# Performance work log

Hardware: AMD Instinct MI355X
Metric: run time of the kernel (lower is better)

The kernel has to match this reference:

```python
import jax, jax.numpy as jnp
import numpy as np
from jax import lax

# NLM hyperparameters (from init_kwargs)
H_PARAM = 7.0 / 255.0          # OpenCV h is in 0-255 intensity units; images are in [0,1]
H2 = H_PARAM * H_PARAM
T = 7                          # template (patch) window size
TH = T // 2
S = 21                         # search window size
SH = S // 2


def setup_inputs() -> dict:
    key = jax.random.key(0)
    x = jax.random.uniform(key, (4, 1, 1024, 1024), dtype=jnp.float32)
    return {"x": x}


def _box_mean(d):
    # mean filter over TxT template window with reflect ('same') padding,
    # done as two separable 1D convolutions.
    k = (jnp.ones((T,), dtype=d.dtype) / T)
    dp = jnp.pad(d, ((0, 0), (0, 0), (TH, TH), (TH, TH)), mode="reflect")
    dn = ("NCHW", "OIHW", "NCHW")
    y = lax.conv_general_dilated(dp, k.reshape(1, 1, T, 1), (1, 1), "VALID", dimension_numbers=dn)
    y = lax.conv_general_dilated(y, k.reshape(1, 1, 1, T), (1, 1), "VALID", dimension_numbers=dn)
    return y


def reference(x):
    B, C, H, W = x.shape
    xc = jnp.clip(x, 0.0, 1.0)
    # reflect-pad by the search radius so every shift is a plain slice
    padded = jnp.pad(xc, ((0, 0), (0, 0), (SH, SH), (SH, SH)), mode="reflect")

    # all SxS = 441 search-window offsets, as padded-array slice origins in [0, 2*SH]
    oy, ox = jnp.meshgrid(jnp.arange(S, dtype=jnp.int32), jnp.arange(S, dtype=jnp.int32), indexing="ij")
    offsets = jnp.stack([oy.reshape(-1), ox.reshape(-1)], axis=-1)  # [441, 2]

    zero = jnp.int32(0)

    def body(carry, off):
        wsum, vsum = carry
        shifted = lax.dynamic_slice(padded, (zero, zero, off[0], off[1]), (B, C, H, W))
        dist = _box_mean((xc - shifted) ** 2)          # mean squared patch difference
        w = jnp.exp(-dist / H2)                        # NLM similarity weight
        return (wsum + w, vsum + w * shifted), None

    init = (jnp.zeros_like(xc), jnp.zeros_like(xc))
    (wsum, vsum), _ = lax.scan(body, init, offsets)
    out = vsum / wsum
    return jnp.clip(out, 0.0, 1.0)
```

## Files before the change

kernel.cpp:

```cpp
#include <hip/hip_runtime.h>
#include <cstddef>


constexpr int TS    = 32;
constexpr int XSTR  = 61;
constexpr int XROWS = 59;
constexpr int XSZ   = XROWS * XSTR;
constexpr int VSTR  = 42;
constexpr int VROWS = 33;
constexpr int VS_SZ = VROWS * VSTR;

__device__ __forceinline__ int refl(int i, int n) {
    i = (i < 0) ? -i : i;
    return (i >= n) ? (2 * n - 2 - i) : i;
}

template<bool FASTROWS>
__device__ __forceinline__ void nlm_body(const float* __restrict__ img,
                                         float* __restrict__ out,
                                         int H, int W, int gx0, int gy0,
                                         float* xs, float* vsh, int tid)
{
    for (int e = tid; e < XSZ; e += 256) {
        int i = e / XSTR, j = e - i * XSTR;
        int jj = (j > 57) ? 57 : j;
        int gy = refl(gy0 - 13 + i, H);
        int gx = refl(gx0 - 13 + jj, W);
        float v = img[(size_t)gy * W + gx];
        xs[e] = fminf(fmaxf(v, 0.0f), 1.0f);
    }
    __syncthreads();

    const bool bv = (tid < 114);
    float u[17];
    int   aS[17];
    int   aB = 0;
    int   wb;
    {
        int t  = bv ? tid : 0;
        int g  = t / 38;
        int cc = t - g * 38;
        int r  = g * 11;
        int mxm10 = refl(gx0 + cc - 3, W) - gx0 + 3;
        if (FASTROWS) {
            aB = r * XSTR + mxm10;
#pragma unroll
            for (int i = 0; i < 17; ++i)
                u[i] = xs[(r + i + 10) * XSTR + mxm10 + 10];
        } else {
#pragma unroll
            for (int i = 0; i < 17; ++i) {
                int my = refl(gy0 + r + i - 3, H) - gy0 + 13;
                u[i]  = xs[my * XSTR + mxm10 + 10];
                aS[i] = (my - 10) * XSTR + mxm10;
            }
        }
        wb = r * VSTR + cc;
    }

    const bool cact = (tid >= 128);
    const int ct = cact ? (tid - 128) : 0;
    const int py = ct >> 2;
    const int c8 = (ct & 3) * 8;
    const int vb = py * VSTR + c8;
    int svC = (py + 3) * XSTR + (c8 + 3);

    int oxB = 0;
    int oxC = 0;

    float p[7];
    float ws[8], ac[8];
#pragma unroll
    for (int k = 0; k < 8; ++k) { ws[k] = 0.f; ac[k] = 0.f; }
    const float K = -(65025.0f / 2401.0f) * 1.4426950408889634f;

    auto bv_step = [&](int buf) {
        if (bv) {
            float* vo = vsh + buf * VS_SZ + wb;
            float q[17];
#pragma unroll
            for (int i = 0; i < 17; ++i) {
                float sh = FASTROWS ? xs[aB + i * XSTR] : xs[aS[i]];
                float d  = u[i] - sh;
                q[i] = d * d;
            }
            float s = ((q[0] + q[1]) + (q[2] + q[3])) + ((q[4] + q[5]) + q[6]);
            vo[0] = s;
#pragma unroll
            for (int k = 1; k < 11; ++k) {
                s += q[k + 6] - q[k - 1];
                vo[k * VSTR] = s;
            }
            int step = (oxB == 20) ? (XSTR - 20) : 1;
            if (FASTROWS) {
                aB += step;
            } else {
#pragma unroll
                for (int i = 0; i < 17; ++i) aS[i] += step;
            }
        }
        oxB = (oxB == 20) ? 0 : oxB + 1;
    };

    auto c_step = [&](int buf) {
        if (cact) {
            if (oxC == 0) {
#pragma unroll
                for (int k = 0; k < 7; ++k) p[k] = xs[svC + k];
            }
            const float2* vp =
                reinterpret_cast<const float2*>(vsh + buf * VS_SZ + vb);
            float2 tA = vp[0], tB = vp[1], tC = vp[2], tD = vp[3];
            float2 tE = vp[4], tF = vp[5], tG = vp[6];
            float p7 = xs[svC + 7 + oxC];
            float h0 = ((tA.x + tA.y) + (tB.x + tB.y)) + ((tC.x + tC.y) + tD.x);
            float h1 = h0 - tA.x + tD.y;
            float h2 = h1 - tA.y + tE.x;
            float h3 = h2 - tB.x + tE.y;
            float h4 = h3 - tB.y + tF.x;
            float h5 = h4 - tC.x + tF.y;
            float h6 = h5 - tC.y + tG.x;
            float h7 = h6 - tD.x + tG.y;
            float w;
            w = __builtin_amdgcn_exp2f(h0 * K); ws[0] += w; ac[0] = fmaf(w, p[0], ac[0]);
            w = __builtin_amdgcn_exp2f(h1 * K); ws[1] += w; ac[1] = fmaf(w, p[1], ac[1]);
            w = __builtin_amdgcn_exp2f(h2 * K); ws[2] += w; ac[2] = fmaf(w, p[2], ac[2]);
            w = __builtin_amdgcn_exp2f(h3 * K); ws[3] += w; ac[3] = fmaf(w, p[3], ac[3]);
            w = __builtin_amdgcn_exp2f(h4 * K); ws[4] += w; ac[4] = fmaf(w, p[4], ac[4]);
            w = __builtin_amdgcn_exp2f(h5 * K); ws[5] += w; ac[5] = fmaf(w, p[5], ac[5]);
            w = __builtin_amdgcn_exp2f(h6 * K); ws[6] += w; ac[6] = fmaf(w, p[6], ac[6]);
            w = __builtin_amdgcn_exp2f(h7 * K); ws[7] += w; ac[7] = fmaf(w, p7,   ac[7]);
#pragma unroll
            for (int k = 0; k < 6; ++k) p[k] = p[k + 1];
            p[6] = p7;
        }
        if (oxC == 20) { oxC = 0; svC += XSTR; } else { ++oxC; }
    };

    bv_step(0);
    __syncthreads();
#pragma unroll 1
    for (int i = 1; i < 441; ++i) {
        bv_step(i & 1);
        c_step(1 - (i & 1));
        __syncthreads();
    }
    c_step(0);

    if (cact) {
        float4 oA, oB;
        oA.x = fminf(fmaxf(ac[0] * __builtin_amdgcn_rcpf(ws[0]), 0.f), 1.f);
        oA.y = fminf(fmaxf(ac[1] * __builtin_amdgcn_rcpf(ws[1]), 0.f), 1.f);
        oA.z = fminf(fmaxf(ac[2] * __builtin_amdgcn_rcpf(ws[2]), 0.f), 1.f);
        oA.w = fminf(fmaxf(ac[3] * __builtin_amdgcn_rcpf(ws[3]), 0.f), 1.f);
        oB.x = fminf(fmaxf(ac[4] * __builtin_amdgcn_rcpf(ws[4]), 0.f), 1.f);
        oB.y = fminf(fmaxf(ac[5] * __builtin_amdgcn_rcpf(ws[5]), 0.f), 1.f);
        oB.z = fminf(fmaxf(ac[6] * __builtin_amdgcn_rcpf(ws[6]), 0.f), 1.f);
        oB.w = fminf(fmaxf(ac[7] * __builtin_amdgcn_rcpf(ws[7]), 0.f), 1.f);
        float* op = &out[((size_t)blockIdx.z * H + (gy0 + py)) * W + (gx0 + c8)];
        *reinterpret_cast<float4*>(op)     = oA;
        *reinterpret_cast<float4*>(op + 4) = oB;
    }
}

__global__ __launch_bounds__(256)
void nlm_kernel(const float* __restrict__ img_all, float* __restrict__ out,
                int H, int W) {
    __shared__ float xs[XSZ];
    __shared__ float vsh[2 * VS_SZ];
    const int tid = threadIdx.x;
    const int gx0 = blockIdx.x * TS;
    const int gy0 = blockIdx.y * TS;
    const float* img = img_all + (size_t)blockIdx.z * H * W;
    if (gy0 - 3 >= 0 && gy0 + 35 < H)
        nlm_body<true>(img, out, H, W, gx0, gy0, xs, vsh, tid);
    else
        nlm_body<false>(img, out, H, W, gx0, gy0, xs, vsh, tid);
}

extern "C" void kernel_launch(void* const* d_in, const int* in_sizes, int n_in,
                              void* d_out, int out_size, void* d_ws, size_t ws_size,
                              hipStream_t stream) {
    const float* x = (const float*)d_in[0];
    float* out = (float*)d_out;
    const int H = 1024, W = 1024;
    const int B = in_sizes[0] / (H * W);
    dim3 grid(W / TS, H / TS, B);
    nlm_kernel<<<grid, dim3(256), 0, stream>>>(x, out, H, W);
}
```

Baseline: 892.7 us.

## Pack vertical patch sums into float2 ops and prescale image to fold exp constant

The interior fast path now computes the vertical box sums for two adjacent columns per thread using 2-wide vector loads and arithmetic, halving the active producer threads and the LDS load instructions. The image is prescaled by sqrt of the exponent constant, which removes a multiply per weight, and the output is unscaled at the end. The XSTR padding changes to 62 to keep the float2 accesses aligned, and the fast path now also requires interior columns. The costs are possible new LDS bank conflicts from the new stride and slight floating-point rounding differences.

```diff
diff --git a/kernel.cpp b/kernel.cpp
--- a/kernel.cpp
+++ b/kernel.cpp
@@ -2,8 +2,10 @@
 #include <cstddef>
 
 
+typedef float v2f __attribute__((ext_vector_type(2)));
+
 constexpr int TS    = 32;
-constexpr int XSTR  = 61;
+constexpr int XSTR  = 62;
 constexpr int XROWS = 59;
 constexpr int XSZ   = XROWS * XSTR;
 constexpr int VSTR  = 42;
@@ -15,45 +17,51 @@
     return (i >= n) ? (2 * n - 2 - i) : i;
 }
 
-template<bool FASTROWS>
+template<bool FAST>
 __device__ __forceinline__ void nlm_body(const float* __restrict__ img,
                                          float* __restrict__ out,
                                          int H, int W, int gx0, int gy0,
                                          float* xs, float* vsh, int tid)
 {
+    const float NK  = (65025.0f / 2401.0f) * 1.4426950408889634f;
+    const float LAM = sqrtf(NK);
+
     for (int e = tid; e < XSZ; e += 256) {
         int i = e / XSTR, j = e - i * XSTR;
         int jj = (j > 57) ? 57 : j;
         int gy = refl(gy0 - 13 + i, H);
         int gx = refl(gx0 - 13 + jj, W);
         float v = img[(size_t)gy * W + gx];
-        xs[e] = fminf(fmaxf(v, 0.0f), 1.0f);
+        xs[e] = fminf(fmaxf(v, 0.0f), 1.0f) * LAM;
     }
     __syncthreads();
 
-    const bool bv = (tid < 114);
-    float u[17];
-    int   aS[17];
-    int   aB = 0;
-    int   wb;
-    {
+    const bool bv = FAST ? (tid < 57) : (tid < 114);
+    v2f   uP[17]; int aB = 0;
+    float uS[17]; int aS[17];
+    int   wb = 0;
+    if constexpr (FAST) {
+        int t  = bv ? tid : 0;
+        int g  = t / 19;
+        int pp = t - g * 19;
+        int r  = g * 11;
+        int cc = 2 * pp;
+        aB = r * XSTR + cc;
+        wb = r * VSTR + cc;
+#pragma unroll
+        for (int i = 0; i < 17; ++i)
+            uP[i] = *reinterpret_cast<const v2f*>(&xs[(r + i + 10) * XSTR + cc + 10]);
+    } else {
         int t  = bv ? tid : 0;
         int g  = t / 38;
         int cc = t - g * 38;
         int r  = g * 11;
         int mxm10 = refl(gx0 + cc - 3, W) - gx0 + 3;
-        if (FASTROWS) {
-            aB = r * XSTR + mxm10;
-#pragma unroll
-            for (int i = 0; i < 17; ++i)
-                u[i] = xs[(r + i + 10) * XSTR + mxm10 + 10];
-        } else {
-#pragma unroll
-            for (int i = 0; i < 17; ++i) {
-                int my = refl(gy0 + r + i - 3, H) - gy0 + 13;
-                u[i]  = xs[my * XSTR + mxm10 + 10];
-                aS[i] = (my - 10) * XSTR + mxm10;
-            }
+#pragma unroll
+        for (int i = 0; i < 17; ++i) {
+            int my = refl(gy0 + r + i - 3, H) - gy0 + 13;
+            uS[i] = xs[my * XSTR + mxm10 + 10];
+            aS[i] = (my - 10) * XSTR + mxm10;
         }
         wb = r * VSTR + cc;
     }
@@ -72,34 +80,51 @@
     float ws[8], ac[8];
 #pragma unroll
     for (int k = 0; k < 8; ++k) { ws[k] = 0.f; ac[k] = 0.f; }
-    const float K = -(65025.0f / 2401.0f) * 1.4426950408889634f;
 
     auto bv_step = [&](int buf) {
         if (bv) {
             float* vo = vsh + buf * VS_SZ + wb;
-            float q[17];
-#pragma unroll
-            for (int i = 0; i < 17; ++i) {
-                float sh = FASTROWS ? xs[aB + i * XSTR] : xs[aS[i]];
-                float d  = u[i] - sh;
-                q[i] = d * d;
-            }
-            float s = ((q[0] + q[1]) + (q[2] + q[3])) + ((q[4] + q[5]) + q[6]);
-            vo[0] = s;
-#pragma unroll
-            for (int k = 1; k < 11; ++k) {
-                s += q[k + 6] - q[k - 1];
-                vo[k * VSTR] = s;
-            }
-            int step = (oxB == 20) ? (XSTR - 20) : 1;
-            if (FASTROWS) {
-                aB += step;
+            if constexpr (FAST) {
+                v2f q[17];
+#pragma unroll
+                for (int i = 0; i < 7; ++i) {
+                    v2f sh = *reinterpret_cast<const v2f*>(&xs[aB + i * XSTR]);
+                    v2f d = uP[i] - sh;
+                    q[i] = d * d;
+                }
+                v2f s = ((q[0] + q[1]) + (q[2] + q[3])) + ((q[4] + q[5]) + q[6]);
+                *reinterpret_cast<v2f*>(vo) = s;
+#pragma unroll
+                for (int k = 1; k < 11; ++k) {
+                    v2f sh = *reinterpret_cast<const v2f*>(&xs[aB + (k + 6) * XSTR]);
+                    v2f d = uP[k + 6] - sh;
+                    q[k + 6] = d * d;
+                    s += q[k + 6] - q[k - 1];
+                    *reinterpret_cast<v2f*>(&vo[k * VSTR]) = s;
+                }
+                aB += (oxB == 20) ? (XSTR - 20) : 1;
             } else {
+                float q[17];
+#pragma unroll
+                for (int i = 0; i < 7; ++i) {
+                    float d = uS[i] - xs[aS[i]];
+                    q[i] = d * d;
+                }
+                float s = ((q[0] + q[1]) + (q[2] + q[3])) + ((q[4] + q[5]) + q[6]);
+                vo[0] = s;
+#pragma unroll
+                for (int k = 1; k < 11; ++k) {
+                    float d = uS[k + 6] - xs[aS[k + 6]];
+                    q[k + 6] = d * d;
+                    s += q[k + 6] - q[k - 1];
+                    vo[k * VSTR] = s;
+                }
+                int step = (oxB == 20) ? (XSTR - 20) : 1;
 #pragma unroll
                 for (int i = 0; i < 17; ++i) aS[i] += step;
             }
         }
-        oxB = (oxB == 20) ? 0 : oxB + 1;
+        oxB = (oxB == 20) ? 0 : (oxB + 1);
     };
 
     auto c_step = [&](int buf) {
@@ -108,10 +133,9 @@
 #pragma unroll
                 for (int k = 0; k < 7; ++k) p[k] = xs[svC + k];
             }
-            const float2* vp =
-                reinterpret_cast<const float2*>(vsh + buf * VS_SZ + vb);
-            float2 tA = vp[0], tB = vp[1], tC = vp[2], tD = vp[3];
-            float2 tE = vp[4], tF = vp[5], tG = vp[6];
+            const v2f* vp = reinterpret_cast<const v2f*>(vsh + buf * VS_SZ + vb);
+            v2f tA = vp[0], tB = vp[1], tC = vp[2], tD = vp[3];
+            v2f tE = vp[4], tF = vp[5], tG = vp[6];
             float p7 = xs[svC + 7 + oxC];
             float h0 = ((tA.x + tA.y) + (tB.x + tB.y)) + ((tC.x + tC.y) + tD.x);
             float h1 = h0 - tA.x + tD.y;
@@ -122,14 +146,14 @@
             float h6 = h5 - tC.y + tG.x;
             float h7 = h6 - tD.x + tG.y;
             float w;
-            w = __builtin_amdgcn_exp2f(h0 * K); ws[0] += w; ac[0] = fmaf(w, p[0], ac[0]);
-            w = __builtin_amdgcn_exp2f(h1 * K); ws[1] += w; ac[1] = fmaf(w, p[1], ac[1]);
-            w = __builtin_amdgcn_exp2f(h2 * K); ws[2] += w; ac[2] = fmaf(w, p[2], ac[2]);
-            w = __builtin_amdgcn_exp2f(h3 * K); ws[3] += w; ac[3] = fmaf(w, p[3], ac[3]);
-            w = __builtin_amdgcn_exp2f(h4 * K); ws[4] += w; ac[4] = fmaf(w, p[4], ac[4]);
-            w = __builtin_amdgcn_exp2f(h5 * K); ws[5] += w; ac[5] = fmaf(w, p[5], ac[5]);
-            w = __builtin_amdgcn_exp2f(h6 * K); ws[6] += w; ac[6] = fmaf(w, p[6], ac[6]);
-            w = __builtin_amdgcn_exp2f(h7 * K); ws[7] += w; ac[7] = fmaf(w, p7,   ac[7]);
+            w = __builtin_amdgcn_exp2f(-h0); ws[0] += w; ac[0] = fmaf(w, p[0], ac[0]);
+            w = __builtin_amdgcn_exp2f(-h1); ws[1] += w; ac[1] = fmaf(w, p[1], ac[1]);
+            w = __builtin_amdgcn_exp2f(-h2); ws[2] += w; ac[2] = fmaf(w, p[2], ac[2]);
+            w = __builtin_amdgcn_exp2f(-h3); ws[3] += w; ac[3] = fmaf(w, p[3], ac[3]);
+            w = __builtin_amdgcn_exp2f(-h4); ws[4] += w; ac[4] = fmaf(w, p[4], ac[4]);
+            w = __builtin_amdgcn_exp2f(-h5); ws[5] += w; ac[5] = fmaf(w, p[5], ac[5]);
+            w = __builtin_amdgcn_exp2f(-h6); ws[6] += w; ac[6] = fmaf(w, p[6], ac[6]);
+            w = __builtin_amdgcn_exp2f(-h7); ws[7] += w; ac[7] = fmaf(w, p7,   ac[7]);
 #pragma unroll
             for (int k = 0; k < 6; ++k) p[k] = p[k + 1];
             p[6] = p7;
@@ -148,15 +172,16 @@
     c_step(0);
 
     if (cact) {
+        const float INVLAM = 1.0f / LAM;
         float4 oA, oB;
-        oA.x = fminf(fmaxf(ac[0] * __builtin_amdgcn_rcpf(ws[0]), 0.f), 1.f);
-        oA.y = fminf(fmaxf(ac[1] * __builtin_amdgcn_rcpf(ws[1]), 0.f), 1.f);
-        oA.z = fminf(fmaxf(ac[2] * __builtin_amdgcn_rcpf(ws[2]), 0.f), 1.f);
-        oA.w = fminf(fmaxf(ac[3] * __builtin_amdgcn_rcpf(ws[3]), 0.f), 1.f);
-        oB.x = fminf(fmaxf(ac[4] * __builtin_amdgcn_rcpf(ws[4]), 0.f), 1.f);
-        oB.y = fminf(fmaxf(ac[5] * __builtin_amdgcn_rcpf(ws[5]), 0.f), 1.f);
-        oB.z = fminf(fmaxf(ac[6] * __builtin_amdgcn_rcpf(ws[6]), 0.f), 1.f);
-        oB.w = fminf(fmaxf(ac[7] * __builtin_amdgcn_rcpf(ws[7]), 0.f), 1.f);
+        oA.x = fminf(fmaxf(ac[0] * __builtin_amdgcn_rcpf(ws[0]) * INVLAM, 0.f), 1.f);
+        oA.y = fminf(fmaxf(ac[1] * __builtin_amdgcn_rcpf(ws[1]) * INVLAM, 0.f), 1.f);
+        oA.z = fminf(fmaxf(ac[2] * __builtin_amdgcn_rcpf(ws[2]) * INVLAM, 0.f), 1.f);
+        oA.w = fminf(fmaxf(ac[3] * __builtin_amdgcn_rcpf(ws[3]) * INVLAM, 0.f), 1.f);
+        oB.x = fminf(fmaxf(ac[4] * __builtin_amdgcn_rcpf(ws[4]) * INVLAM, 0.f), 1.f);
+        oB.y = fminf(fmaxf(ac[5] * __builtin_amdgcn_rcpf(ws[5]) * INVLAM, 0.f), 1.f);
+        oB.z = fminf(fmaxf(ac[6] * __builtin_amdgcn_rcpf(ws[6]) * INVLAM, 0.f), 1.f);
+        oB.w = fminf(fmaxf(ac[7] * __builtin_amdgcn_rcpf(ws[7]) * INVLAM, 0.f), 1.f);
         float* op = &out[((size_t)blockIdx.z * H + (gy0 + py)) * W + (gx0 + c8)];
         *reinterpret_cast<float4*>(op)     = oA;
         *reinterpret_cast<float4*>(op + 4) = oB;
@@ -166,13 +191,13 @@
 __global__ __launch_bounds__(256)
 void nlm_kernel(const float* __restrict__ img_all, float* __restrict__ out,
                 int H, int W) {
-    __shared__ float xs[XSZ];
-    __shared__ float vsh[2 * VS_SZ];
+    __shared__ __align__(16) float xs[XSZ];
+    __shared__ __align__(16) float vsh[2 * VS_SZ];
     const int tid = threadIdx.x;
     const int gx0 = blockIdx.x * TS;
     const int gy0 = blockIdx.y * TS;
     const float* img = img_all + (size_t)blockIdx.z * H * W;
-    if (gy0 - 3 >= 0 && gy0 + 35 < H)
+    if (gy0 - 3 >= 0 && gy0 + 35 < H && gx0 - 3 >= 0 && gx0 + 34 < W)
         nlm_body<true>(img, out, H, W, gx0, gy0, xs, vsh, tid);
     else
         nlm_body<false>(img, out, H, W, gx0, gy0, xs, vsh, tid);
```

Measured after the change: 2.200 ms. 146% more time.

## Store row-sum intermediates as fp16 and alternate producer/consumer wave roles by block parity

Applied to the files above, without the earlier changes.

Intermediate vertical patch sums in shared memory are now stored as half precision, halving LDS footprint and bandwidth for the producer-consumer exchange. Block parity swaps which thread range does the column-sum producer work versus the weight/accumulate consumer work, so that work is spread across different waves/SIMDs between neighbouring blocks. The xs stride shrinks to 59, the horizontal running sums are restarted at h4 to limit error, and loads are split from arithmetic to aid scheduling. fp16 rounding of squared-difference sums adds precision risk to the exponent weights.

```diff
diff --git a/kernel.cpp b/kernel.cpp
--- a/kernel.cpp
+++ b/kernel.cpp
@@ -2,8 +2,11 @@
 #include <cstddef>
 
 
+typedef _Float16 hf;
+typedef _Float16 hf2 __attribute__((ext_vector_type(2)));
+
 constexpr int TS    = 32;
-constexpr int XSTR  = 61;
+constexpr int XSTR  = 59;
 constexpr int XROWS = 59;
 constexpr int XSZ   = XROWS * XSTR;
 constexpr int VSTR  = 42;
@@ -15,11 +18,13 @@
     return (i >= n) ? (2 * n - 2 - i) : i;
 }
 
-template<bool FASTROWS>
+template<bool FAST>
 __device__ __forceinline__ void nlm_body(const float* __restrict__ img,
                                          float* __restrict__ out,
                                          int H, int W, int gx0, int gy0,
-                                         float* xs, float* vsh, int tid)
+                                         float* __restrict__ xs,
+                                         hf* __restrict__ vsh,
+                                         int tid, int parity)
 {
     for (int e = tid; e < XSZ; e += 256) {
         int i = e / XSTR, j = e - i * XSTR;
@@ -31,18 +36,19 @@
     }
     __syncthreads();
 
-    const bool bv = (tid < 114);
+    const int  bvt = parity ? (tid - 142) : tid;
+    const bool bv  = ((unsigned)bvt < 114u);
     float u[17];
+    int   aB = 0;
     int   aS[17];
-    int   aB = 0;
-    int   wb;
+    int   wb = 0;
     {
-        int t  = bv ? tid : 0;
+        int t  = bv ? bvt : 0;
         int g  = t / 38;
         int cc = t - g * 38;
         int r  = g * 11;
         int mxm10 = refl(gx0 + cc - 3, W) - gx0 + 3;
-        if (FASTROWS) {
+        if constexpr (FAST) {
             aB = r * XSTR + mxm10;
 #pragma unroll
             for (int i = 0; i < 17; ++i)
@@ -58,8 +64,8 @@
         wb = r * VSTR + cc;
     }
 
-    const bool cact = (tid >= 128);
-    const int ct = cact ? (tid - 128) : 0;
+    const bool cact = parity ? (tid < 128) : (tid >= 128);
+    const int ct = cact ? (parity ? tid : (tid - 128)) : 0;
     const int py = ct >> 2;
     const int c8 = (ct & 3) * 8;
     const int vb = py * VSTR + c8;
@@ -76,30 +82,39 @@
 
     auto bv_step = [&](int buf) {
         if (bv) {
-            float* vo = vsh + buf * VS_SZ + wb;
+            hf* vo = vsh + buf * VS_SZ + wb;
             float q[17];
+            if constexpr (FAST) {
+#pragma unroll
+                for (int i = 0; i < 17; ++i)
+                    q[i] = xs[aB + i * XSTR];
+            } else {
+#pragma unroll
+                for (int i = 0; i < 17; ++i)
+                    q[i] = xs[aS[i]];
+            }
 #pragma unroll
             for (int i = 0; i < 17; ++i) {
-                float sh = FASTROWS ? xs[aB + i * XSTR] : xs[aS[i]];
-                float d  = u[i] - sh;
+                float d = u[i] - q[i];
                 q[i] = d * d;
             }
-            float s = ((q[0] + q[1]) + (q[2] + q[3])) + ((q[4] + q[5]) + q[6]);
-            vo[0] = s;
-#pragma unroll
-            for (int k = 1; k < 11; ++k) {
-                s += q[k + 6] - q[k - 1];
-                vo[k * VSTR] = s;
-            }
-            int step = (oxB == 20) ? (XSTR - 20) : 1;
-            if (FASTROWS) {
-                aB += step;
+            float s[11];
+            s[0] = ((q[0] + q[1]) + (q[2] + q[3])) + ((q[4] + q[5]) + q[6]);
+#pragma unroll
+            for (int k = 1; k < 11; ++k)
+                s[k] = s[k - 1] + (q[k + 6] - q[k - 1]);
+#pragma unroll
+            for (int k = 0; k < 11; ++k)
+                vo[k * VSTR] = (hf)s[k];
+            if constexpr (FAST) {
+                aB += (oxB == 20) ? (XSTR - 20) : 1;
             } else {
+                int step = (oxB == 20) ? (XSTR - 20) : 1;
 #pragma unroll
                 for (int i = 0; i < 17; ++i) aS[i] += step;
             }
         }
-        oxB = (oxB == 20) ? 0 : oxB + 1;
+        oxB = (oxB == 20) ? 0 : (oxB + 1);
     };
 
     auto c_step = [&](int buf) {
@@ -108,19 +123,25 @@
 #pragma unroll
                 for (int k = 0; k < 7; ++k) p[k] = xs[svC + k];
             }
-            const float2* vp =
-                reinterpret_cast<const float2*>(vsh + buf * VS_SZ + vb);
-            float2 tA = vp[0], tB = vp[1], tC = vp[2], tD = vp[3];
-            float2 tE = vp[4], tF = vp[5], tG = vp[6];
+            const hf2* vp = reinterpret_cast<const hf2*>(vsh + buf * VS_SZ + vb);
+            hf2 A = vp[0], B = vp[1], Cv = vp[2], D = vp[3];
+            hf2 E = vp[4], F = vp[5], G = vp[6];
+            float a0 = (float)A.x,  a1 = (float)A.y;
+            float b0 = (float)B.x,  b1 = (float)B.y;
+            float c0 = (float)Cv.x, c1 = (float)Cv.y;
+            float d0 = (float)D.x,  d1 = (float)D.y;
+            float e0 = (float)E.x,  e1 = (float)E.y;
+            float f0 = (float)F.x,  f1 = (float)F.y;
+            float g0 = (float)G.x,  g1 = (float)G.y;
             float p7 = xs[svC + 7 + oxC];
-            float h0 = ((tA.x + tA.y) + (tB.x + tB.y)) + ((tC.x + tC.y) + tD.x);
-            float h1 = h0 - tA.x + tD.y;
-            float h2 = h1 - tA.y + tE.x;
-            float h3 = h2 - tB.x + tE.y;
-            float h4 = h3 - tB.y + tF.x;
-            float h5 = h4 - tC.x + tF.y;
-            float h6 = h5 - tC.y + tG.x;
-            float h7 = h6 - tD.x + tG.y;
+            float h0 = ((a0 + a1) + (b0 + b1)) + ((c0 + c1) + d0);
+            float h1 = h0 - a0 + d1;
+            float h2 = h1 - a1 + e0;
+            float h3 = h2 - b0 + e1;
+            float h4 = ((c0 + c1) + (d0 + d1)) + ((e0 + e1) + f0);
+            float h5 = h4 - c0 + f1;
+            float h6 = h5 - c1 + g0;
+            float h7 = h6 - d0 + g1;
             float w;
             w = __builtin_amdgcn_exp2f(h0 * K); ws[0] += w; ac[0] = fmaf(w, p[0], ac[0]);
             w = __builtin_amdgcn_exp2f(h1 * K); ws[1] += w; ac[1] = fmaf(w, p[1], ac[1]);
@@ -166,16 +187,17 @@
 __global__ __launch_bounds__(256)
 void nlm_kernel(const float* __restrict__ img_all, float* __restrict__ out,
                 int H, int W) {
-    __shared__ float xs[XSZ];
-    __shared__ float vsh[2 * VS_SZ];
+    __shared__ __align__(16) float xs[XSZ];
+    __shared__ __align__(16) hf vsh[2 * VS_SZ];
     const int tid = threadIdx.x;
     const int gx0 = blockIdx.x * TS;
     const int gy0 = blockIdx.y * TS;
+    const int parity = (blockIdx.x ^ blockIdx.y) & 1;
     const float* img = img_all + (size_t)blockIdx.z * H * W;
     if (gy0 - 3 >= 0 && gy0 + 35 < H)
-        nlm_body<true>(img, out, H, W, gx0, gy0, xs, vsh, tid);
+        nlm_body<true>(img, out, H, W, gx0, gy0, xs, vsh, tid, parity);
     else
-        nlm_body<false>(img, out, H, W, gx0, gy0, xs, vsh, tid);
+        nlm_body<false>(img, out, H, W, gx0, gy0, xs, vsh, tid, parity);
 }
 
 extern "C" void kernel_launch(void* const* d_in, const int* in_sizes, int n_in,
```

Result: slower. 1.070 ms (+19.8%).
